# Kernel optimization log

Hardware: AMD Instinct MI355X
Metric: run time of the kernel (lower is better)

Reference implementation:

```python
import jax, jax.numpy as jnp
import numpy as np

N_AST = 200000
N_TEST = 10000
H = 128
NUM_AST_LABELS = 128
AST_CONTENT = 256
NUM_CLASSES = 2
N_LAYERS = 5
E_AA, E_AT, E_TA = 2000000, 500000, 500000


def seg_mean(msg, dst, n):
    # mean aggregation of edge messages per destination node
    s = jax.ops.segment_sum(msg, dst, num_segments=n)
    d = jax.ops.segment_sum(jnp.ones((dst.shape[0], 1), msg.dtype), dst, num_segments=n)
    return s / jnp.maximum(d, 1.0)


def gcn_layer(h_ast, h_test, src_aa, dst_aa, src_at, dst_at, src_ta, dst_ta,
              W_aa, W_at, W_ta, b_ast, b_test):
    # transform-then-aggregate per canonical edge type, sum over edge types per dst ntype
    m_aa = seg_mean((h_ast @ W_aa)[src_aa], dst_aa, N_AST)
    m_ta = seg_mean((h_test @ W_ta)[src_ta], dst_ta, N_AST)
    new_ast = jax.nn.relu(m_aa + m_ta + b_ast)
    m_at = seg_mean((h_ast @ W_at)[src_at], dst_at, N_TEST)
    new_test = jax.nn.relu(m_at + b_test)
    return new_ast, new_test


def setup_inputs() -> dict:
    key = jax.random.key(0)
    ks = jax.random.split(key, 16)
    Hh = H // 2
    inp = {
        "ast_label": jax.random.randint(ks[0], (N_AST,), 0, NUM_AST_LABELS),
        "ast_content": jax.random.normal(ks[1], (N_AST, AST_CONTENT), jnp.float32),
        "src_aa": jax.random.randint(ks[2], (E_AA,), 0, N_AST, jnp.int32),
        "dst_aa": jax.random.randint(ks[3], (E_AA,), 0, N_AST, jnp.int32),
        "src_at": jax.random.randint(ks[4], (E_AT,), 0, N_AST, jnp.int32),
        "dst_at": jax.random.randint(ks[5], (E_AT,), 0, N_TEST, jnp.int32),
        "src_ta": jax.random.randint(ks[6], (E_TA,), 0, N_TEST, jnp.int32),
        "dst_ta": jax.random.randint(ks[7], (E_TA,), 0, N_AST, jnp.int32),
        "n_test": N_TEST,
        "ast_label_emb": jax.random.normal(ks[8], (NUM_AST_LABELS, Hh), jnp.float32) * 0.1,
        "ast_content_W": jax.random.normal(ks[9], (AST_CONTENT, Hh), jnp.float32) * (1.0 / np.sqrt(AST_CONTENT)),
        "ast_content_b": jax.random.normal(ks[10], (Hh,), jnp.float32) * 0.1,
        "test_embedding": jax.random.normal(ks[11], (H,), jnp.float32),
        "W_aa": jax.random.normal(ks[12], (N_LAYERS, H, H), jnp.float32) * (1.0 / np.sqrt(H)),
        "W_at": jax.random.normal(ks[13], (N_LAYERS, H, H), jnp.float32) * (1.0 / np.sqrt(H)),
        "W_ta": jax.random.normal(ks[14], (N_LAYERS, H, H), jnp.float32) * (1.0 / np.sqrt(H)),
        "b_ast": jnp.zeros((N_LAYERS, H), jnp.float32),
        "b_test": jnp.zeros((N_LAYERS, H), jnp.float32),
        "dec_W": jax.random.normal(ks[15], (H, NUM_CLASSES), jnp.float32) * (1.0 / np.sqrt(H)),
        "dec_b": jnp.zeros((NUM_CLASSES,), jnp.float32),
    }
    return inp


def reference(ast_label, ast_content, src_aa, dst_aa, src_at, dst_at, src_ta, dst_ta,
              n_test, ast_label_emb, ast_content_W, ast_content_b, test_embedding,
              W_aa, W_at, W_ta, b_ast, b_test, dec_W, dec_b):
    # hetero node encoding: ast = [embedding(label) || linear(content)], test = broadcast learned vector
    h_ast = jnp.concatenate(
        [ast_label_emb[ast_label], ast_content @ ast_content_W + ast_content_b], axis=-1)
    h_test = jnp.broadcast_to(test_embedding[None, :], (n_test, H))

    def layer(i, ha, ht):
        return gcn_layer(ha, ht, src_aa, dst_aa, src_at, dst_at, src_ta, dst_ta,
                         W_aa[i], W_at[i], W_ta[i], b_ast[i], b_test[i])

    h_ast, h_test = layer(0, h_ast, h_test)
    res_a, res_t = h_ast, h_test
    h_ast, h_test = layer(1, h_ast, h_test)
    h_ast, h_test = res_a + h_ast, res_t + h_test
    h_ast, h_test = layer(2, h_ast, h_test)
    res_a, res_t = h_ast, h_test
    h_ast, h_test = layer(3, h_ast, h_test)
    h_ast, h_test = res_a + h_ast, res_t + h_test
    h_ast, h_test = layer(4, h_ast, h_test)

    logits = h_ast @ dec_W + dec_b  # ast_decode_node_func with num_classes>1 -> softmax
    pred = jax.nn.softmax(logits, axis=1)
    return logits, pred
```

## Files before the change

### kernel.cpp

```cpp
#include <hip/hip_runtime.h>

#define N_ASTN 200000
#define N_TESTN 10000
#define HDIM 128
#define E_AA_N 2000000
#define E_AT_N 500000
#define E_TA_N 500000
#define NBA 196
#define NBT 10

typedef __bf16 bf16x8 __attribute__((ext_vector_type(8)));
typedef float f32x4 __attribute__((ext_vector_type(4)));
typedef float f32x2 __attribute__((ext_vector_type(2)));

static __device__ __forceinline__ float bflo(unsigned u) {
    union { unsigned x; float f; } c; c.x = u << 16; return c.f;
}
static __device__ __forceinline__ float bfhi(unsigned u) {
    union { unsigned x; float f; } c; c.x = u & 0xffff0000u; return c.f;
}
static __device__ __forceinline__ unsigned short f2bf(float f) {
    union { float f; unsigned u; } c; c.f = f;
    unsigned u = c.u;
    return (unsigned short)((u + 0x7fffu + ((u >> 16) & 1u)) >> 16);
}
static __device__ __forceinline__ unsigned pack2(float a, float b) {
    return (unsigned)f2bf(a) | ((unsigned)f2bf(b) << 16);
}
static __device__ __forceinline__ f32x2 unpk(unsigned u) {
    union { unsigned q[2]; f32x2 v; } t;
    t.q[0] = u << 16;
    t.q[1] = u & 0xffff0000u;
    return t.v;
}

#define ACC4(S, U) \
    S[0] += unpk((U).x); S[1] += unpk((U).y); \
    S[2] += unpk((U).z); S[3] += unpk((U).w);


__global__ void detect_k(const unsigned short* __restrict__ p, int* __restrict__ flag) {
    __shared__ int cnt;
    if (threadIdx.x == 0) cnt = 0;
    __syncthreads();
    int local = 0;
    for (int i = threadIdx.x; i < 8192; i += 256) {
        unsigned e = ((unsigned)p[i] >> 7) & 0xFFu;
        if (e >= 158u) local++;
    }
    atomicAdd(&cnt, local);
    __syncthreads();
    if (threadIdx.x == 0) *flag = (cnt > 64) ? 1 : 0;
}


struct ConvSpec {
    const void* src[11];
    int off[11];
    int total;
};

__global__ void conv_params_k(ConvSpec spec, const int* __restrict__ flag,
                              unsigned short* __restrict__ dst) {
    int f32 = *flag;
    int i = blockIdx.x * blockDim.x + threadIdx.x;
    int stride = gridDim.x * blockDim.x;
    for (; i < spec.total; i += stride) {
        int s = 10;
        for (int k = 1; k < 11; k++) {
            if (i < spec.off[k]) { s = k - 1; break; }
        }
        int j = i - spec.off[s];
        unsigned short v;
        if (f32) v = f2bf(((const float*)spec.src[s])[j]);
        else     v = ((const unsigned short*)spec.src[s])[j];
        dst[i] = v;
    }
}


__global__ void count3_k(const int* __restrict__ dAA, const int* __restrict__ dTA,
                         const int* __restrict__ dAT,
                         int* __restrict__ cAA, int* __restrict__ cTA, int* __restrict__ cAT) {
    int i = blockIdx.x * blockDim.x + threadIdx.x;
    int stride = gridDim.x * blockDim.x;
    const int T = E_AA_N + E_TA_N + E_AT_N;
    for (; i < T; i += stride) {
        if (i < E_AA_N) {
            unsigned d = (unsigned)dAA[i];
            if (d < (unsigned)N_ASTN) atomicAdd(&cAA[d], 1);
        } else if (i < E_AA_N + E_TA_N) {
            unsigned d = (unsigned)dTA[i - E_AA_N];
            if (d < (unsigned)N_ASTN) atomicAdd(&cTA[d], 1);
        } else {
            unsigned d = (unsigned)dAT[i - (E_AA_N + E_TA_N)];
            if (d < (unsigned)N_TESTN) atomicAdd(&cAT[d], 1);
        }
    }
}

__global__ void scan_bsum3(const int* __restrict__ cA, const int* __restrict__ cT,
                           const int* __restrict__ cX,
                           int* __restrict__ bA, int* __restrict__ bT, int* __restrict__ bX) {
    __shared__ int lds[256];
    int b = blockIdx.x, tid = threadIdx.x;
    const int* in; int n; int* bsum; int bb;
    if (b < NBA)            { in = cA; n = N_ASTN + 1;  bsum = bA; bb = b; }
    else if (b < 2 * NBA)   { in = cT; n = N_ASTN + 1;  bsum = bT; bb = b - NBA; }
    else                    { in = cX; n = N_TESTN + 1; bsum = bX; bb = b - 2 * NBA; }
    int base = bb * 1024 + tid * 4;
    int s = 0;
#pragma unroll
    for (int j = 0; j < 4; j++) { int i = base + j; if (i < n) s += in[i]; }
    lds[tid] = s; __syncthreads();
    for (int off = 128; off; off >>= 1) {
        if (tid < off) lds[tid] += lds[tid + off];
        __syncthreads();
    }
    if (tid == 0) bsum[bb] = lds[0];
}

__global__ void scan_top3(int* __restrict__ bA, int* __restrict__ bT, int* __restrict__ bX) {
    __shared__ int lds[256];
    int b = blockIdx.x, tid = threadIdx.x;
    int* bsum; int nb;
    if (b == 0)      { bsum = bA; nb = NBA; }
    else if (b == 1) { bsum = bT; nb = NBA; }
    else             { bsum = bX; nb = NBT; }
    int v = (tid < nb) ? bsum[tid] : 0;
    lds[tid] = v; __syncthreads();
    for (int off = 1; off < 256; off <<= 1) {
        int t = (tid >= off) ? lds[tid - off] : 0;
        __syncthreads();
        lds[tid] += t;
        __syncthreads();
    }
    if (tid < nb) bsum[tid] = lds[tid] - v;
}

__global__ void scan_final3(const int* __restrict__ cA, const int* __restrict__ cT,
                            const int* __restrict__ cX,
                            const int* __restrict__ bA, const int* __restrict__ bT,
                            const int* __restrict__ bX,
                            int* __restrict__ ipA, int* __restrict__ ipT, int* __restrict__ ipX) {
    __shared__ int lds[256];
    int b = blockIdx.x, tid = threadIdx.x;
    const int* in; int n; const int* bsum; int* out; int bb;
    if (b < NBA)          { in = cA; n = N_ASTN + 1;  bsum = bA; out = ipA; bb = b; }
    else if (b < 2 * NBA) { in = cT; n = N_ASTN + 1;  bsum = bT; out = ipT; bb = b - NBA; }
    else                  { in = cX; n = N_TESTN + 1; bsum = bX; out = ipX; bb = b - 2 * NBA; }
    int base = bb * 1024 + tid * 4;
    int v[4]; int s = 0;
#pragma unroll
    for (int j = 0; j < 4; j++) { int i = base + j; v[j] = (i < n) ? in[i] : 0; s += v[j]; }
    lds[tid] = s; __syncthreads();
    for (int off = 1; off < 256; off <<= 1) {
        int t = (tid >= off) ? lds[tid - off] : 0;
        __syncthreads();
        lds[tid] += t;
        __syncthreads();
    }
    int texcl = lds[tid] - s;
    int run = bsum[bb] + texcl;
#pragma unroll
    for (int j = 0; j < 4; j++) { int i = base + j; if (i < n) out[i] = run; run += v[j]; }
}

__global__ void fill3_k(const int* __restrict__ sAA, const int* __restrict__ dAA,
                        const int* __restrict__ ipAA, int* __restrict__ curAA, int* __restrict__ eAA,
                        const int* __restrict__ sTA, const int* __restrict__ dTA,
                        const int* __restrict__ ipTA, int* __restrict__ curTA, int* __restrict__ eTA,
                        const int* __restrict__ sAT, const int* __restrict__ dAT,
                        const int* __restrict__ ipAT, int* __restrict__ curAT, int* __restrict__ eAT) {
    int i = blockIdx.x * blockDim.x + threadIdx.x;
    int stride = gridDim.x * blockDim.x;
    const int T = E_AA_N + E_TA_N + E_AT_N;
    for (; i < T; i += stride) {
        const int* src; const int* dst; const int* ip; int* cur; int* ed; int nN, nE, j;
        if (i < E_AA_N) {
            j = i; src = sAA; dst = dAA; ip = ipAA; cur = curAA; ed = eAA;
            nN = N_ASTN; nE = E_AA_N;
        } else if (i < E_AA_N + E_TA_N) {
            j = i - E_AA_N; src = sTA; dst = dTA; ip = ipTA; cur = curTA; ed = eTA;
            nN = N_ASTN; nE = E_TA_N;
        } else {
            j = i - (E_AA_N + E_TA_N); src = sAT; dst = dAT; ip = ipAT; cur = curAT; ed = eAT;
            nN = N_TESTN; nE = E_AT_N;
        }
        unsigned d = (unsigned)dst[j];
        if (d >= (unsigned)nN) continue;
        unsigned pos = (unsigned)(ip[d] + atomicAdd(&cur[d], 1));
        if (pos < (unsigned)nE) ed[pos] = src[j];
    }
}


__global__ void encode_emb(const int* __restrict__ label, const unsigned* __restrict__ embU,
                           unsigned* __restrict__ hAU) {
    int idx = blockIdx.x * blockDim.x + threadIdx.x;
    int node = idx >> 5, c = idx & 31;
    int lb = label[node] & 127;
    hAU[node * 64 + c] = embU[lb * 32 + c];
}

__global__ void init_test(const unsigned* __restrict__ tEmbU, unsigned* __restrict__ hTU) {
    int idx = blockIdx.x * blockDim.x + threadIdx.x;
    int node = idx >> 6, c = idx & 63;
    hTU[node * 64 + c] = tEmbU[c];
}


template<int NST>
__global__ void __launch_bounds__(256) gemm_rowblk(
    const void* __restrict__ Araw, const __bf16* __restrict__ W,
    const __bf16* __restrict__ bias, __bf16* __restrict__ C,
    int M, int K, int lda, int ldc, const int* __restrict__ flagp)
{
    __shared__ __bf16 sW[16384];
    int a_f32 = flagp ? *flagp : 0;
    int tid = threadIdx.x;
    int nkb = K >> 5;
    const int N = NST * 16;
    int ngroups = nkb * NST * 64;
    for (int g = tid; g < ngroups; g += 256) {
        int l = g & 63;
        int sk = g >> 6;
        int s = sk % NST, kb = sk / NST;
        int krow = kb * 32 + ((l >> 4) << 3);
        int col = s * 16 + (l & 15);
        bf16x8 tmp;
#pragma unroll
        for (int j = 0; j < 8; j++) tmp[j] = W[(krow + j) * N + col];
        *(bf16x8*)(&sW[g * 8]) = tmp;
    }
    __syncthreads();
    int wave = tid >> 6, lane = tid & 63;
    int mrow = lane & 15, koff = (lane >> 4) << 3;
    int tilesM = M >> 4;
    for (int mt = blockIdx.x * 4 + wave; mt < tilesM; mt += gridDim.x * 4) {
        int m0 = mt << 4;
        f32x4 acc[NST];
#pragma unroll
        for (int s = 0; s < NST; s++) acc[s] = (f32x4){0.f, 0.f, 0.f, 0.f};
        for (int kb = 0; kb < nkb; kb++) {
            bf16x8 a;
            if (a_f32) {
                const float* Af = (const float*)Araw + (size_t)(m0 + mrow) * lda + koff + kb * 32;
                f32x4 x0 = *(const f32x4*)Af;
                f32x4 x1 = *(const f32x4*)(Af + 4);
#pragma unroll
                for (int j = 0; j < 4; j++) { a[j] = (__bf16)x0[j]; a[4 + j] = (__bf16)x1[j]; }
            } else {
                const __bf16* Ab = (const __bf16*)Araw + (size_t)(m0 + mrow) * lda + koff + kb * 32;
                a = *(const bf16x8*)Ab;
            }
#pragma unroll
            for (int s = 0; s < NST; s++) {
                bf16x8 b = *(const bf16x8*)(&sW[((kb * NST + s) * 64 + lane) * 8]);
                acc[s] = __builtin_amdgcn_mfma_f32_16x16x32_bf16(a, b, acc[s], 0, 0, 0);
            }
        }
        int r0 = m0 + ((lane >> 4) << 2);
#pragma unroll
        for (int s = 0; s < NST; s++) {
            int col = s * 16 + (lane & 15);
            float bv = bias ? (float)bias[col] : 0.f;
#pragma unroll
            for (int i = 0; i < 4; i++)
                C[(size_t)(r0 + i) * ldc + col] = (__bf16)(acc[s][i] + bv);
        }
    }
}


__global__ void __launch_bounds__(256) test_transform(
    const __bf16* __restrict__ A, const __bf16* __restrict__ W,
    const __bf16* __restrict__ bias, __bf16* __restrict__ C,
    int M, int resflag)
{
    __shared__ __bf16 sW[16384];
    int tid = threadIdx.x;
    for (int g = tid; g < 2048; g += 256) {
        int l = g & 63;
        int sk = g >> 6;
        int s = sk & 7, kb = sk >> 3;
        int krow = kb * 32 + ((l >> 4) << 3);
        int col = s * 16 + (l & 15);
        bf16x8 tmp;
#pragma unroll
        for (int j = 0; j < 8; j++) tmp[j] = W[(krow + j) * 128 + col];
        *(bf16x8*)(&sW[g * 8]) = tmp;
    }
    __syncthreads();
    int wave = tid >> 6, lane = tid & 63;
    int mrow = lane & 15, koff = (lane >> 4) << 3;
    int total = (M >> 4) * 8;
    for (int t = blockIdx.x * 4 + wave; t < total; t += gridDim.x * 4) {
        int s = t & 7;
        int m0 = (t >> 3) << 4;
        f32x4 acc = {0.f, 0.f, 0.f, 0.f};
#pragma unroll
        for (int kb = 0; kb < 4; kb++) {
            bf16x8 a = *(const bf16x8*)(A + (size_t)(m0 + mrow) * 128 + koff + kb * 32);
            bf16x8 b = *(const bf16x8*)(&sW[((kb * 8 + s) * 64 + lane) * 8]);
            acc = __builtin_amdgcn_mfma_f32_16x16x32_bf16(a, b, acc, 0, 0, 0);
        }
        int col = s * 16 + (lane & 15);
        float bv = (float)bias[col];
        int r0 = m0 + ((lane >> 4) << 2);
#pragma unroll
        for (int i = 0; i < 4; i++) {
            float v = fmaxf(acc[i] + bv, 0.f);
            if (resflag) v += (float)C[(size_t)(r0 + i) * 128 + col];
            C[(size_t)(r0 + i) * 128 + col] = (__bf16)v;
        }
    }
}


template<int DECODE>
__global__ void __launch_bounds__(256) ast_update(
    const uint4* __restrict__ TAq, const uint4* __restrict__ TTq,
    const int* __restrict__ ipA, const int* __restrict__ eA,
    const int* __restrict__ ipT, const int* __restrict__ eT,
    const uint4* __restrict__ biasq, unsigned* __restrict__ h,
    int n, int resflag,
    const uint4* __restrict__ decWq, const unsigned* __restrict__ decbU,
    void* __restrict__ outp, const int* __restrict__ flagp)
{
    int node = (blockIdx.x * blockDim.x + threadIdx.x) >> 4;
    int l = threadIdx.x & 15;
    if (node >= n) return;
    const char* TAb = (const char*)TAq;
    const char* TTb = (const char*)TTq;
    unsigned loff = (unsigned)l << 4;

    int a0 = ipA[node], a1 = ipA[node + 1];
    int t0 = ipT[node], t1 = ipT[node + 1];

    f32x2 sa[4] = {{0.f,0.f},{0.f,0.f},{0.f,0.f},{0.f,0.f}};
    {
        int e = a0;
        for (; e + 3 < a1; e += 4) {
            unsigned o0 = ((unsigned)eA[e]     << 8) + loff;
            unsigned o1 = ((unsigned)eA[e + 1] << 8) + loff;
            unsigned o2 = ((unsigned)eA[e + 2] << 8) + loff;
            unsigned o3 = ((unsigned)eA[e + 3] << 8) + loff;
            uint4 u0 = *(const uint4*)(TAb + o0);
            uint4 u1 = *(const uint4*)(TAb + o1);
            uint4 u2 = *(const uint4*)(TAb + o2);
            uint4 u3 = *(const uint4*)(TAb + o3);
            ACC4(sa, u0) ACC4(sa, u1) ACC4(sa, u2) ACC4(sa, u3)
        }
        for (; e < a1; e++) {
            unsigned o0 = ((unsigned)eA[e] << 8) + loff;
            uint4 u0 = *(const uint4*)(TAb + o0);
            ACC4(sa, u0)
        }
    }
    f32x2 st[4] = {{0.f,0.f},{0.f,0.f},{0.f,0.f},{0.f,0.f}};
    {
        int e = t0;
        for (; e + 1 < t1; e += 2) {
            unsigned o0 = ((unsigned)eT[e]     << 8) + loff;
            unsigned o1 = ((unsigned)eT[e + 1] << 8) + loff;
            uint4 u0 = *(const uint4*)(TTb + o0);
            uint4 u1 = *(const uint4*)(TTb + o1);
            ACC4(st, u0) ACC4(st, u1)
        }
        if (e < t1) {
            unsigned o0 = ((unsigned)eT[e] << 8) + loff;
            uint4 u0 = *(const uint4*)(TTb + o0);
            ACC4(st, u0)
        }
    }
    int da = a1 - a0; if (da < 1) da = 1;
    int dt = t1 - t0; if (dt < 1) dt = 1;
    float inva = 1.0f / (float)da, invt = 1.0f / (float)dt;
    uint4 ub = biasq[l];
    float v[8];
    v[0] = sa[0].x * inva + st[0].x * invt + bflo(ub.x);
    v[1] = sa[0].y * inva + st[0].y * invt + bfhi(ub.x);
    v[2] = sa[1].x * inva + st[1].x * invt + bflo(ub.y);
    v[3] = sa[1].y * inva + st[1].y * invt + bfhi(ub.y);
    v[4] = sa[2].x * inva + st[2].x * invt + bflo(ub.z);
    v[5] = sa[2].y * inva + st[2].y * invt + bfhi(ub.z);
    v[6] = sa[3].x * inva + st[3].x * invt + bflo(ub.w);
    v[7] = sa[3].y * inva + st[3].y * invt + bfhi(ub.w);
#pragma unroll
    for (int j = 0; j < 8; j++) v[j] = fmaxf(v[j], 0.f);

    if (DECODE) {
        uint4 w0 = decWq[l * 2], w1 = decWq[l * 2 + 1];
        float p0 = 0.f, p1 = 0.f;
        p0 += v[0] * bflo(w0.x); p1 += v[0] * bfhi(w0.x);
        p0 += v[1] * bflo(w0.y); p1 += v[1] * bfhi(w0.y);
        p0 += v[2] * bflo(w0.z); p1 += v[2] * bfhi(w0.z);
        p0 += v[3] * bflo(w0.w); p1 += v[3] * bfhi(w0.w);
        p0 += v[4] * bflo(w1.x); p1 += v[4] * bfhi(w1.x);
        p0 += v[5] * bflo(w1.y); p1 += v[5] * bfhi(w1.y);
        p0 += v[6] * bflo(w1.z); p1 += v[6] * bfhi(w1.z);
        p0 += v[7] * bflo(w1.w); p1 += v[7] * bfhi(w1.w);
#pragma unroll
        for (int off = 1; off < 16; off <<= 1) {
            p0 += __shfl_xor(p0, off);
            p1 += __shfl_xor(p1, off);
        }
        if (l == 0) {
            unsigned db = decbU[0];
            float l0 = p0 + bflo(db);
            float l1 = p1 + bfhi(db);
            float m = fmaxf(l0, l1);
            float e0 = __expf(l0 - m), e1 = __expf(l1 - m);
            float invs = 1.0f / (e0 + e1);
            if (*flagp) {
                float* o = (float*)outp;
                o[node * 2 + 0] = l0;
                o[node * 2 + 1] = l1;
                o[2 * N_ASTN + node * 2 + 0] = e0 * invs;
                o[2 * N_ASTN + node * 2 + 1] = e1 * invs;
            } else {
                unsigned short* o = (unsigned short*)outp;
                o[node * 2 + 0] = f2bf(l0);
                o[node * 2 + 1] = f2bf(l1);
                o[2 * N_ASTN + node * 2 + 0] = f2bf(e0 * invs);
                o[2 * N_ASTN + node * 2 + 1] = f2bf(e1 * invs);
            }
        }
        return;
    }

    uint4* hq = (uint4*)h;
    if (resflag) {
        uint4 r = hq[(size_t)node * 16 + l];
        v[0] += bflo(r.x); v[1] += bfhi(r.x);
        v[2] += bflo(r.y); v[3] += bfhi(r.y);
        v[4] += bflo(r.z); v[5] += bfhi(r.z);
        v[6] += bflo(r.w); v[7] += bfhi(r.w);
    }
    uint4 o;
    o.x = pack2(v[0], v[1]); o.y = pack2(v[2], v[3]);
    o.z = pack2(v[4], v[5]); o.w = pack2(v[6], v[7]);
    hq[(size_t)node * 16 + l] = o;
}


__global__ void __launch_bounds__(256) agg_at_k(
    const uint4* __restrict__ Hq,
    const int* __restrict__ ip, const int* __restrict__ ed,
    uint4* __restrict__ outq, int n)
{
    int node = (blockIdx.x * blockDim.x + threadIdx.x) >> 4;
    int l = threadIdx.x & 15;
    if (node >= n) return;
    const char* Hb = (const char*)Hq;
    unsigned loff = (unsigned)l << 4;
    f32x2 sa[4] = {{0.f,0.f},{0.f,0.f},{0.f,0.f},{0.f,0.f}};
    int a0 = ip[node], a1 = ip[node + 1];
    {
        int e = a0;
        for (; e + 3 < a1; e += 4) {
            unsigned o0 = ((unsigned)ed[e]     << 8) + loff;
            unsigned o1 = ((unsigned)ed[e + 1] << 8) + loff;
            unsigned o2 = ((unsigned)ed[e + 2] << 8) + loff;
            unsigned o3 = ((unsigned)ed[e + 3] << 8) + loff;
            uint4 u0 = *(const uint4*)(Hb + o0);
            uint4 u1 = *(const uint4*)(Hb + o1);
            uint4 u2 = *(const uint4*)(Hb + o2);
            uint4 u3 = *(const uint4*)(Hb + o3);
            ACC4(sa, u0) ACC4(sa, u1) ACC4(sa, u2) ACC4(sa, u3)
        }
        for (; e < a1; e++) {
            unsigned o0 = ((unsigned)ed[e] << 8) + loff;
            uint4 u0 = *(const uint4*)(Hb + o0);
            ACC4(sa, u0)
        }
    }
    int da = a1 - a0; if (da < 1) da = 1;
    float inv = 1.0f / (float)da;
    uint4 o;
    o.x = pack2(sa[0].x * inv, sa[0].y * inv);
    o.y = pack2(sa[1].x * inv, sa[1].y * inv);
    o.z = pack2(sa[2].x * inv, sa[2].y * inv);
    o.w = pack2(sa[3].x * inv, sa[3].y * inv);
    outq[(size_t)node * 16 + l] = o;
}


extern "C" void kernel_launch(void* const* d_in, const int* in_sizes, int n_in,
                              void* d_out, int out_size, void* d_ws, size_t ws_size,
                              hipStream_t stream) {
    const int* ast_label = (const int*)d_in[0];
    const void* ast_content = d_in[1];
    const int* src_aa = (const int*)d_in[2];
    const int* dst_aa = (const int*)d_in[3];
    const int* src_at = (const int*)d_in[4];
    const int* dst_at = (const int*)d_in[5];
    const int* src_ta = (const int*)d_in[6];
    const int* dst_ta = (const int*)d_in[7];

    char* ws = (char*)d_ws;
    size_t off = 0;
    auto alloc = [&](size_t bytes) {
        char* p = ws + off;
        off += (bytes + 255) & ~(size_t)255;
        return p;
    };
    int* flag = (int*)alloc(256);
    const int P_EMB = 0, P_CW = 8192, P_CB = 24576, P_TEMB = 24640, P_WAA = 24768,
              P_WAT = 106688, P_WTA = 188608, P_BAST = 270528, P_BTEST = 271168,
              P_DECW = 271808, P_DECB = 272064, P_TOTAL = 272066;
    __bf16* params = (__bf16*)alloc((size_t)P_TOTAL * 2);
    __bf16* hA = (__bf16*)alloc((size_t)N_ASTN * HDIM * 2);
    __bf16* TA = (__bf16*)alloc((size_t)N_ASTN * HDIM * 2);
    __bf16* hT = (__bf16*)alloc((size_t)N_TESTN * HDIM * 2);
    __bf16* TT = (__bf16*)alloc((size_t)N_TESTN * HDIM * 2);
    int* ip_aa = (int*)alloc((size_t)(N_ASTN + 1) * 4);
    int* ip_ta = (int*)alloc((size_t)(N_ASTN + 1) * 4);
    int* ip_at = (int*)alloc((size_t)(N_TESTN + 1) * 4);
    int* e_aa = (int*)alloc((size_t)E_AA_N * 4);
    int* e_ta = (int*)alloc((size_t)E_TA_N * 4);
    int* e_at = (int*)alloc((size_t)E_AT_N * 4);
    char* zbase = alloc(((size_t)(N_ASTN + 1 + N_ASTN) * 2 + (N_TESTN + 1 + N_TESTN)) * 4);
    int* cnt_aa = (int*)zbase;
    int* cur_aa = cnt_aa + (N_ASTN + 1);
    int* cnt_ta = cur_aa + N_ASTN;
    int* cur_ta = cnt_ta + (N_ASTN + 1);
    int* cnt_at = cur_ta + N_ASTN;
    int* cur_at = cnt_at + (N_TESTN + 1);
    size_t zbytes = ((size_t)(N_ASTN + 1 + N_ASTN) * 2 + (N_TESTN + 1 + N_TESTN)) * 4;
    int* bsumA = (int*)alloc(256 * 4);
    int* bsumT = (int*)alloc(256 * 4);
    int* bsumX = (int*)alloc(256 * 4);
    __bf16* aggAT = (__bf16*)zbase;

    if (ws_size < off) {
        hipMemsetAsync(d_out, 0, (size_t)out_size * 2, stream);
        return;
    }

    detect_k<<<1, 256, 0, stream>>>((const unsigned short*)ast_content, flag);
    ConvSpec spec;
    spec.src[0] = d_in[9];  spec.off[0] = P_EMB;
    spec.src[1] = d_in[10]; spec.off[1] = P_CW;
    spec.src[2] = d_in[11]; spec.off[2] = P_CB;
    spec.src[3] = d_in[12]; spec.off[3] = P_TEMB;
    spec.src[4] = d_in[13]; spec.off[4] = P_WAA;
    spec.src[5] = d_in[14]; spec.off[5] = P_WAT;
    spec.src[6] = d_in[15]; spec.off[6] = P_WTA;
    spec.src[7] = d_in[16]; spec.off[7] = P_BAST;
    spec.src[8] = d_in[17]; spec.off[8] = P_BTEST;
    spec.src[9] = d_in[18]; spec.off[9] = P_DECW;
    spec.src[10] = d_in[19]; spec.off[10] = P_DECB;
    spec.total = P_TOTAL;
    conv_params_k<<<256, 256, 0, stream>>>(spec, flag, (unsigned short*)params);

    hipMemsetAsync(zbase, 0, zbytes, stream);

    count3_k<<<3072, 256, 0, stream>>>(dst_aa, dst_ta, dst_at, cnt_aa, cnt_ta, cnt_at);
    scan_bsum3<<<2 * NBA + NBT, 256, 0, stream>>>(cnt_aa, cnt_ta, cnt_at, bsumA, bsumT, bsumX);
    scan_top3<<<3, 256, 0, stream>>>(bsumA, bsumT, bsumX);
    scan_final3<<<2 * NBA + NBT, 256, 0, stream>>>(cnt_aa, cnt_ta, cnt_at,
                                                   bsumA, bsumT, bsumX,
                                                   ip_aa, ip_ta, ip_at);
    fill3_k<<<3072, 256, 0, stream>>>(src_aa, dst_aa, ip_aa, cur_aa, e_aa,
                                      src_ta, dst_ta, ip_ta, cur_ta, e_ta,
                                      src_at, dst_at, ip_at, cur_at, e_at);

    encode_emb<<<N_ASTN * 32 / 256, 256, 0, stream>>>(ast_label, (const unsigned*)(params + P_EMB),
                                                      (unsigned*)hA);
    gemm_rowblk<4><<<1568, 256, 0, stream>>>(ast_content, params + P_CW, params + P_CB,
                                             hA + 64, N_ASTN, 256, 256, HDIM, flag);
    init_test<<<N_TESTN * 64 / 256, 256, 0, stream>>>((const unsigned*)(params + P_TEMB),
                                                      (unsigned*)hT);

    const uint4* decWq = (const uint4*)(params + P_DECW);
    const unsigned* decbU = (const unsigned*)(params + P_DECB);
    const int resflags[5] = {0, 1, 0, 1, 0};
    for (int l = 0; l < 5; l++) {
        const __bf16* Waa = params + P_WAA + (size_t)l * HDIM * HDIM;
        const __bf16* Wat = params + P_WAT + (size_t)l * HDIM * HDIM;
        const __bf16* Wta = params + P_WTA + (size_t)l * HDIM * HDIM;
        gemm_rowblk<8><<<160, 256, 0, stream>>>(hT, Wta, nullptr, TT, N_TESTN, HDIM, HDIM, HDIM, nullptr);
        agg_at_k<<<N_TESTN / 16, 256, 0, stream>>>(
            (const uint4*)hA, ip_at, e_at, (uint4*)aggAT, N_TESTN);
        gemm_rowblk<8><<<1568, 256, 0, stream>>>(hA, Waa, nullptr, TA, N_ASTN, HDIM, HDIM, HDIM, nullptr);
        test_transform<<<256, 256, 0, stream>>>(
            aggAT, Wat, params + P_BTEST + (size_t)l * HDIM, hT, N_TESTN, resflags[l]);
        if (l < 4) {
            ast_update<0><<<N_ASTN / 16, 256, 0, stream>>>(
                (const uint4*)TA, (const uint4*)TT, ip_aa, e_aa, ip_ta, e_ta,
                (const uint4*)(params + P_BAST + (size_t)l * HDIM), (unsigned*)hA,
                N_ASTN, resflags[l], nullptr, nullptr, nullptr, nullptr);
        } else {
            ast_update<1><<<N_ASTN / 16, 256, 0, stream>>>(
                (const uint4*)TA, (const uint4*)TT, ip_aa, e_aa, ip_ta, e_ta,
                (const uint4*)(params + P_BAST + (size_t)l * HDIM), (unsigned*)hA,
                N_ASTN, 0, decWq, decbU, d_out, flag);
        }
    }
}
```

Baseline: 1.491 ms.

## Build CSR in two passes with coarse destination buckets before the fine scatter

```diff
diff --git a/kernel.cpp b/kernel.cpp
--- a/kernel.cpp
+++ b/kernel.cpp
@@ -8,6 +8,9 @@
 #define E_TA_N 500000
 #define NBA 196
 #define NBT 10
+#define BSHIFT 7
+#define NBK_A 1563
+#define NBK_T 79
 
 typedef __bf16 bf16x8 __attribute__((ext_vector_type(8)));
 typedef float f32x4 __attribute__((ext_vector_type(4)));
@@ -166,31 +169,70 @@
     for (int j = 0; j < 4; j++) { int i = base + j; if (i < n) out[i] = run; run += v[j]; }
 }
 
-__global__ void fill3_k(const int* __restrict__ sAA, const int* __restrict__ dAA,
-                        const int* __restrict__ ipAA, int* __restrict__ curAA, int* __restrict__ eAA,
-                        const int* __restrict__ sTA, const int* __restrict__ dTA,
-                        const int* __restrict__ ipTA, int* __restrict__ curTA, int* __restrict__ eTA,
-                        const int* __restrict__ sAT, const int* __restrict__ dAT,
-                        const int* __restrict__ ipAT, int* __restrict__ curAT, int* __restrict__ eAT) {
+
+__global__ void bucket3_k(
+    const int* __restrict__ sAA, const int* __restrict__ dAA,
+    const int* __restrict__ ipAA, int* __restrict__ bcAA, uint2* __restrict__ prAA,
+    const int* __restrict__ sTA, const int* __restrict__ dTA,
+    const int* __restrict__ ipTA, int* __restrict__ bcTA, uint2* __restrict__ prTA,
+    const int* __restrict__ sAT, const int* __restrict__ dAT,
+    const int* __restrict__ ipAT, int* __restrict__ bcAT, uint2* __restrict__ prAT)
+{
     int i = blockIdx.x * blockDim.x + threadIdx.x;
     int stride = gridDim.x * blockDim.x;
     const int T = E_AA_N + E_TA_N + E_AT_N;
     for (; i < T; i += stride) {
-        const int* src; const int* dst; const int* ip; int* cur; int* ed; int nN, nE, j;
+        const int *src, *dst, *ip; int* bc; uint2* pr; int nN, nE, j;
         if (i < E_AA_N) {
-            j = i; src = sAA; dst = dAA; ip = ipAA; cur = curAA; ed = eAA;
+            j = i; src = sAA; dst = dAA; ip = ipAA; bc = bcAA; pr = prAA;
             nN = N_ASTN; nE = E_AA_N;
         } else if (i < E_AA_N + E_TA_N) {
-            j = i - E_AA_N; src = sTA; dst = dTA; ip = ipTA; cur = curTA; ed = eTA;
+            j = i - E_AA_N; src = sTA; dst = dTA; ip = ipTA; bc = bcTA; pr = prTA;
             nN = N_ASTN; nE = E_TA_N;
         } else {
-            j = i - (E_AA_N + E_TA_N); src = sAT; dst = dAT; ip = ipAT; cur = curAT; ed = eAT;
+            j = i - (E_AA_N + E_TA_N); src = sAT; dst = dAT; ip = ipAT; bc = bcAT; pr = prAT;
             nN = N_TESTN; nE = E_AT_N;
         }
         unsigned d = (unsigned)dst[j];
         if (d >= (unsigned)nN) continue;
+        int b = (int)(d >> BSHIFT);
+        unsigned pos = (unsigned)(ip[b << BSHIFT] + atomicAdd(&bc[b], 1));
+        if (pos < (unsigned)nE) {
+            uint2 p; p.x = (unsigned)src[j]; p.y = d;
+            pr[pos] = p;
+        }
+    }
+}
+
+
+__global__ void fillfine3_k(
+    const uint2* __restrict__ prAA, const int* __restrict__ ipAA,
+    int* __restrict__ curAA, int* __restrict__ eAA,
+    const uint2* __restrict__ prTA, const int* __restrict__ ipTA,
+    int* __restrict__ curTA, int* __restrict__ eTA,
+    const uint2* __restrict__ prAT, const int* __restrict__ ipAT,
+    int* __restrict__ curAT, int* __restrict__ eAT)
+{
+    int totAA = ipAA[N_ASTN];
+    int totTA = ipTA[N_ASTN];
+    int totAT = ipAT[N_TESTN];
+    int i = blockIdx.x * blockDim.x + threadIdx.x;
+    int stride = gridDim.x * blockDim.x;
+    const int T = E_AA_N + E_TA_N + E_AT_N;
+    for (; i < T; i += stride) {
+        const uint2* pr; const int* ip; int* cur; int* ed; int nE, j, tot;
+        if (i < E_AA_N) {
+            j = i; pr = prAA; ip = ipAA; cur = curAA; ed = eAA; nE = E_AA_N; tot = totAA;
+        } else if (i < E_AA_N + E_TA_N) {
+            j = i - E_AA_N; pr = prTA; ip = ipTA; cur = curTA; ed = eTA; nE = E_TA_N; tot = totTA;
+        } else {
+            j = i - (E_AA_N + E_TA_N); pr = prAT; ip = ipAT; cur = curAT; ed = eAT; nE = E_AT_N; tot = totAT;
+        }
+        if (j >= tot) continue;
+        uint2 p = pr[j];
+        unsigned d = p.y;
         unsigned pos = (unsigned)(ip[d] + atomicAdd(&cur[d], 1));
-        if (pos < (unsigned)nE) ed[pos] = src[j];
+        if (pos < (unsigned)nE) ed[pos] = (int)p.x;
     }
 }
 
@@ -521,14 +563,22 @@
     int* e_aa = (int*)alloc((size_t)E_AA_N * 4);
     int* e_ta = (int*)alloc((size_t)E_TA_N * 4);
     int* e_at = (int*)alloc((size_t)E_AT_N * 4);
-    char* zbase = alloc(((size_t)(N_ASTN + 1 + N_ASTN) * 2 + (N_TESTN + 1 + N_TESTN)) * 4);
+    uint2* pr_aa = (uint2*)alloc((size_t)E_AA_N * 8);
+    uint2* pr_ta = (uint2*)alloc((size_t)E_TA_N * 8);
+    uint2* pr_at = (uint2*)alloc((size_t)E_AT_N * 8);
+    char* zbase = alloc(((size_t)(N_ASTN + 1 + N_ASTN) * 2 + (N_TESTN + 1 + N_TESTN)
+                         + NBK_A * 2 + NBK_T) * 4);
     int* cnt_aa = (int*)zbase;
     int* cur_aa = cnt_aa + (N_ASTN + 1);
     int* cnt_ta = cur_aa + N_ASTN;
     int* cur_ta = cnt_ta + (N_ASTN + 1);
     int* cnt_at = cur_ta + N_ASTN;
     int* cur_at = cnt_at + (N_TESTN + 1);
-    size_t zbytes = ((size_t)(N_ASTN + 1 + N_ASTN) * 2 + (N_TESTN + 1 + N_TESTN)) * 4;
+    int* bc_aa = cur_at + N_TESTN;
+    int* bc_ta = bc_aa + NBK_A;
+    int* bc_at = bc_ta + NBK_A;
+    size_t zbytes = ((size_t)(N_ASTN + 1 + N_ASTN) * 2 + (N_TESTN + 1 + N_TESTN)
+                     + NBK_A * 2 + NBK_T) * 4;
     int* bsumA = (int*)alloc(256 * 4);
     int* bsumT = (int*)alloc(256 * 4);
     int* bsumX = (int*)alloc(256 * 4);
@@ -563,9 +613,12 @@
     scan_final3<<<2 * NBA + NBT, 256, 0, stream>>>(cnt_aa, cnt_ta, cnt_at,
                                                    bsumA, bsumT, bsumX,
                                                    ip_aa, ip_ta, ip_at);
-    fill3_k<<<3072, 256, 0, stream>>>(src_aa, dst_aa, ip_aa, cur_aa, e_aa,
-                                      src_ta, dst_ta, ip_ta, cur_ta, e_ta,
-                                      src_at, dst_at, ip_at, cur_at, e_at);
+    bucket3_k<<<3072, 256, 0, stream>>>(src_aa, dst_aa, ip_aa, bc_aa, pr_aa,
+                                        src_ta, dst_ta, ip_ta, bc_ta, pr_ta,
+                                        src_at, dst_at, ip_at, bc_at, pr_at);
+    fillfine3_k<<<3072, 256, 0, stream>>>(pr_aa, ip_aa, cur_aa, e_aa,
+                                          pr_ta, ip_ta, cur_ta, e_ta,
+                                          pr_at, ip_at, cur_at, e_at);
 
     encode_emb<<<N_ASTN * 32 / 256, 256, 0, stream>>>(ast_label, (const unsigned*)(params + P_EMB),
                                                       (unsigned*)hA);
```

New measurement: 1.972 ms. 32.3% more time.
